# Performance work log

Measured on AMD Instinct MI355X. Metric: run time of the kernel, lower is better.

Reference implementation:

```python
import jax, jax.numpy as jnp
import numpy as np

B, S, D, H, FF = 2, 2048, 1024, 16, 4096
DK = D // H
MAX_SEQ_LEN = 2048
THETA = 10000.0
EPS = 1e-5


def _linear_init(key, out_f, in_f):
    std = (2.0 / (in_f + out_f)) ** 0.5
    return std * jax.random.truncated_normal(key, -3.0, 3.0, (out_f, in_f), dtype=jnp.float32)


def setup_inputs() -> dict:
    key = jax.random.key(0)
    ks = jax.random.split(key, 9)
    x = jax.random.normal(ks[0], (B, S, D), dtype=jnp.float32)
    token_positions = jnp.broadcast_to(jnp.arange(S, dtype=jnp.int32)[None, :], (B, S))
    return {
        "x": x,
        "wq": _linear_init(ks[1], D, D),
        "wk": _linear_init(ks[2], D, D),
        "wv": _linear_init(ks[3], D, D),
        "wo": _linear_init(ks[4], D, D),
        "w1": _linear_init(ks[5], FF, D),
        "w2": _linear_init(ks[6], D, FF),
        "w3": _linear_init(ks[7], FF, D),
        "g1": jnp.ones((D,), dtype=jnp.float32),
        "g2": jnp.ones((D,), dtype=jnp.float32),
        "token_positions": token_positions,
    }


def _rmsnorm(x, g):
    x32 = x.astype(jnp.float32)
    ms = jnp.sqrt(jnp.mean(x32 * x32, axis=-1, keepdims=True) + EPS)
    return ((x32 / ms) * g).astype(x.dtype)


def _rope(x, pos):
    # x: (B, H, S, DK); pos: (B, S)
    inv_freq = 1.0 / THETA ** (jnp.arange(0, DK, 2, dtype=jnp.float32) / DK)  # (DK/2,)
    freqs = pos.astype(jnp.float32)[..., None] * inv_freq  # (B, S, DK/2)
    cos = jnp.cos(freqs)[:, None, :, :]  # (B, 1, S, DK/2) broadcast over heads
    sin = jnp.sin(freqs)[:, None, :, :]
    x_real = x[..., 0::2]
    x_imag = x[..., 1::2]
    rot_real = x_real * cos - x_imag * sin
    rot_imag = x_real * sin + x_imag * cos
    return jnp.stack([rot_real, rot_imag], axis=-1).reshape(x.shape)


def reference(x, wq, wk, wv, wo, w1, w2, w3, g1, g2, token_positions):
    # --- attention sublayer ---
    h = _rmsnorm(x, g1)
    def proj(w):
        y = jnp.einsum('bsd,ed->bse', h, w)
        return y.reshape(B, S, H, DK).transpose(0, 2, 1, 3)  # (B,H,S,DK)
    Q = _rope(proj(wq), token_positions)
    K = _rope(proj(wk), token_positions)
    V = proj(wv)
    scores = jnp.einsum('bhqd,bhkd->bhqk', Q, K)  # (B,H,S,S) full matrix (naive)
    causal = jnp.tril(jnp.ones((S, S), dtype=bool))
    scores = jnp.where(causal, scores, -jnp.inf) / (DK ** 0.5)
    probs = jax.nn.softmax(scores, axis=-1)
    attn = jnp.einsum('bhqk,bhkd->bhqd', probs, V)
    attn = attn.transpose(0, 2, 1, 3).reshape(B, S, D)
    attn = jnp.einsum('bsd,ed->bse', attn, wo)
    y = x + attn
    # --- SwiGLU FFN sublayer ---
    h2 = _rmsnorm(y, g2)
    a = jnp.einsum('bsd,fd->bsf', h2, w1)
    gate = jnp.einsum('bsd,fd->bsf', h2, w3)
    ff = jnp.einsum('bsf,df->bsd', a * jax.nn.sigmoid(a) * gate, w2)
    return y + ff
```

## Files before the change

kernel.cpp:

```cpp
#include <hip/hip_runtime.h>
#include <hip/hip_bf16.h>

#define B_ 2
#define S_ 2048
#define D_ 1024
#define H_ 16
#define DK_ 64
#define FF_ 4096
#define M_ (B_ * S_)

typedef unsigned short u16;
typedef __bf16 bf16x8 __attribute__((ext_vector_type(8)));
typedef float f32x4 __attribute__((ext_vector_type(4)));
typedef u16 u16x4 __attribute__((ext_vector_type(4)));
typedef u16 u16x8 __attribute__((ext_vector_type(8)));

__device__ __forceinline__ u16 f2bf(float f) {
  __bf16 b = (__bf16)f;
  return __builtin_bit_cast(u16, b);
}
__device__ __forceinline__ float bf2f(u16 u) {
  __bf16 b = __builtin_bit_cast(__bf16, u);
  return (float)b;
}

__device__ __forceinline__ void async_lds16(const void* g, void* l) {
  __builtin_amdgcn_global_load_lds(
      (const __attribute__((address_space(1))) unsigned int*)g,
      (__attribute__((address_space(3))) unsigned int*)l, 16, 0, 0);
}

__device__ __forceinline__ void raw_barrier() {
  asm volatile("s_barrier" ::: "memory");
}
#define VMCNT_WAIT(n) asm volatile("s_waitcnt vmcnt(" #n ")" ::: "memory")

__global__ __launch_bounds__(256) void f2b_all(
    const float* __restrict__ wq, const float* __restrict__ wk,
    const float* __restrict__ wv, const float* __restrict__ wo,
    const float* __restrict__ w1, const float* __restrict__ w2,
    const float* __restrict__ w3, u16* __restrict__ wqkvb,
    u16* __restrict__ wob, u16* __restrict__ w1b, u16* __restrict__ w2b,
    u16* __restrict__ w3b) {
  int i4 = blockIdx.x * 256 + threadIdx.x;
  const float* src;
  u16* dst;
  int off;
  if (i4 < 262144) { src = wq; dst = wqkvb; off = i4; }
  else if (i4 < 524288) { src = wk; dst = wqkvb + 1048576; off = i4 - 262144; }
  else if (i4 < 786432) { src = wv; dst = wqkvb + 2097152; off = i4 - 524288; }
  else if (i4 < 1048576) { src = wo; dst = wob; off = i4 - 786432; }
  else if (i4 < 2097152) { src = w1; dst = w1b; off = i4 - 1048576; }
  else if (i4 < 3145728) { src = w2; dst = w2b; off = i4 - 2097152; }
  else { src = w3; dst = w3b; off = i4 - 3145728; }
  float4 v = ((const float4*)src)[off];
  u16x4 o;
  o[0] = f2bf(v.x); o[1] = f2bf(v.y); o[2] = f2bf(v.z); o[3] = f2bf(v.w);
  *(u16x4*)(dst + (size_t)off * 4) = o;
}

__global__ __launch_bounds__(256) void rmsnorm_k(const float* __restrict__ X,
                                                 const float* __restrict__ G,
                                                 u16* __restrict__ Out) {
  const int row = blockIdx.x, tid = threadIdx.x;
  const float4 xv = *(const float4*)(X + (size_t)row * D_ + tid * 4);
  float ss = xv.x * xv.x + xv.y * xv.y + xv.z * xv.z + xv.w * xv.w;
#pragma unroll
  for (int off = 1; off < 64; off <<= 1) ss += __shfl_xor(ss, off);
  __shared__ float red[4];
  if ((tid & 63) == 0) red[tid >> 6] = ss;
  __syncthreads();
  const float tot = red[0] + red[1] + red[2] + red[3];
  const float sc = rsqrtf(tot * (1.0f / D_) + 1e-5f);
  const float4 gv = *(const float4*)(G + tid * 4);
  u16x4 o;
  o[0] = f2bf(xv.x * sc * gv.x);
  o[1] = f2bf(xv.y * sc * gv.y);
  o[2] = f2bf(xv.z * sc * gv.z);
  o[3] = f2bf(xv.w * sc * gv.w);
  *(u16x4*)(Out + (size_t)row * D_ + tid * 4) = o;
}

__global__ __launch_bounds__(256) void rope2_k(unsigned int* __restrict__ Qb,
                                               unsigned int* __restrict__ Kb,
                                               const int* __restrict__ pos) {
  int idx = blockIdx.x * 256 + threadIdx.x;
  unsigned int* buf = Qb;
  float scale = 0.125f;
  if (idx >= 2097152) { buf = Kb; scale = 1.f; idx -= 2097152; }
  const int row = idx >> 9, p = idx & 511;
  const int i = p & 31;
  unsigned int v = buf[(size_t)row * 512 + p];
  const float xr = bf2f((u16)(v & 0xffffu));
  const float xi = bf2f((u16)(v >> 16));
  const float ang =
      (float)pos[row] * __expf(-(float)i * (9.210340371976184f / 32.0f));
  float sn, cs;
  sincosf(ang, &sn, &cs);
  const float orr = (xr * cs - xi * sn) * scale;
  const float oii = (xr * sn + xi * cs) * scale;
  buf[(size_t)row * 512 + p] =
      (unsigned int)f2bf(orr) | ((unsigned int)f2bf(oii) << 16);
}

__global__ __launch_bounds__(256) void transpose_v(const u16* __restrict__ V,
                                                   u16* __restrict__ Vt) {
  __shared__ __align__(16) u16 tile[32][64];
  const int tid = threadIdx.x;
  const int s0 = blockIdx.x * 32, bh = blockIdx.y, b = bh >> 4, h = bh & 15;
  {
    const int sr = tid >> 3, c = tid & 7;
    *(u16x8*)&tile[sr][c * 8] =
        *(const u16x8*)(V + (size_t)(b * S_ + s0 + sr) * D_ + h * DK_ + c * 8);
  }
  __syncthreads();
  {
    const int dk = tid >> 2, cs = tid & 3;
    u16x8 vv;
#pragma unroll
    for (int j = 0; j < 8; ++j) vv[j] = tile[cs * 8 + j][dk];
    *(u16x8*)(Vt + (size_t)(bh * DK_ + dk) * S_ + s0 + cs * 8) = vv;
  }
}

template <int EPI>
__global__ __launch_bounds__(512) void gemm8ph(const u16* __restrict__ A,
                                               const u16* __restrict__ Bw,
                                               void* __restrict__ Cout,
                                               const void* __restrict__ auxp,
                                               int N, int K) {
  constexpr int BM = 256, BN = 256, BK = 64;
  constexpr int CPR = BK / 8;
  constexpr int ACH = BM * CPR;
  __shared__ __align__(16) u16 As[2][BM * BK];
  __shared__ __align__(16) u16 Bs[2][BN * BK];
  const int tid = threadIdx.x, l = tid & 63, w = tid >> 6;
  const int gx = gridDim.x;
  const int nwg = gx * (int)gridDim.y;
  const int id = blockIdx.y * gx + blockIdx.x;
  const int swz = (id & 7) * (nwg >> 3) + (id >> 3);
  const int m0 = (swz / gx) * BM, n0 = (swz % gx) * BN;
  const int wm = (w >> 2) * 128, wn = (w & 3) * 64;
  const int lr = l & 15, lg = l >> 4;

  f32x4 acc[8][4] = {};

  auto STAGE_PART = [&](int bf, int k0, int i0, int i1) {
    for (int i = i0; i < i1; ++i) {
      const int s = i * 512 + tid;
      const int base = i * 512 + w * 64;
      if (base < ACH) {
        const int r = s / CPR, ch = s % CPR;
        async_lds16(A + (size_t)(m0 + r) * K + k0 + ((ch ^ (r & 7)) * 8),
                    (char*)As[bf] + base * 16);
      } else {
        const int s2 = s - ACH;
        const int r = s2 / CPR, ch = s2 % CPR;
        async_lds16(Bw + (size_t)(n0 + r) * K + k0 + ((ch ^ (r & 7)) * 8),
                    (char*)Bs[bf] + (base - ACH) * 16);
      }
    }
  };

  STAGE_PART(0, 0, 0, 8);
  VMCNT_WAIT(0);
  raw_barrier();
  int cur = 0;
  for (int k0 = 0; k0 < K; k0 += BK) {
    const bool more = (k0 + BK) < K;
    bf16x8 bfr[4];
#pragma unroll
    for (int ph = 0; ph < 4; ++ph) {
      const int kk = ph >> 1, iq = ph & 1;
      if (iq == 0) {
#pragma unroll
        for (int j = 0; j < 4; ++j) {
          const int row = wn + j * 16 + lr;
          bfr[j] = *(const bf16x8*)&Bs[cur][row * BK +
                                            (((kk * 4 + lg) ^ (row & 7)) * 8)];
        }
      }
      bf16x8 af[4];
#pragma unroll
      for (int i = 0; i < 4; ++i) {
        const int row = wm + (iq * 4 + i) * 16 + lr;
        af[i] = *(const bf16x8*)&As[cur][row * BK +
                                         (((kk * 4 + lg) ^ (row & 7)) * 8)];
      }
      if (more) {
        if (ph == 0) STAGE_PART(cur ^ 1, k0 + BK, 0, 3);
        else if (ph == 1) STAGE_PART(cur ^ 1, k0 + BK, 3, 6);
        else if (ph == 2) STAGE_PART(cur ^ 1, k0 + BK, 6, 8);
      }
      raw_barrier();
      __builtin_amdgcn_s_setprio(1);
#pragma unroll
      for (int i = 0; i < 4; ++i)
#pragma unroll
        for (int j = 0; j < 4; ++j)
          acc[iq * 4 + i][j] = __builtin_amdgcn_mfma_f32_16x16x32_bf16(
              af[i], bfr[j], acc[iq * 4 + i][j], 0, 0, 0);
      __builtin_amdgcn_s_setprio(0);
      if (ph < 3) raw_barrier();
    }
    if (more) {
      VMCNT_WAIT(0);
      raw_barrier();
    }
    cur ^= 1;
  }

#pragma unroll
  for (int i = 0; i < 8; ++i) {
#pragma unroll
    for (int j = 0; j < 4; ++j) {
#pragma unroll
      for (int t = 0; t < 4; ++t) {
        const int grow = m0 + wm + i * 16 + lg * 4 + t;
        const int gcol = n0 + wn + j * 16 + lr;
        const float v = acc[i][j][t];
        if (EPI == 0) {
          ((u16*)Cout)[(size_t)grow * N + gcol] = f2bf(v);
        } else if (EPI == 2) {
          const size_t idx = (size_t)grow * N + gcol;
          const float av = bf2f(((const u16*)auxp)[idx]);
          const float sw = av / (1.f + __expf(-av));
          ((u16*)Cout)[idx] = f2bf(sw * v);
        } else {
          u16* base = (u16*)Cout + (size_t)(gcol >> 10) * ((size_t)M_ * D_);
          base[(size_t)grow * D_ + (gcol & 1023)] = f2bf(v);
        }
      }
    }
  }
}

template <int BM, int BN, int BK, int EPI>
__global__ __launch_bounds__(512) void gemm2ph(const u16* __restrict__ A,
                                               const u16* __restrict__ Bw,
                                               void* __restrict__ Cout,
                                               const void* __restrict__ auxp,
                                               int N, int K) {
  constexpr int CPR = BK / 8;
  constexpr int ACH = BM * CPR;
  constexpr int TCH = (BM + BN) * CPR;
  constexpr int MR = BM / 32, NR = BN / 64;
  static_assert(TCH / 512 == 8, "vmcnt(8) assumes 8 loads/thread per STAGE");
  __shared__ __align__(16) u16 As[2][BM * BK];
  __shared__ __align__(16) u16 Bs[2][BN * BK];
  const int tid = threadIdx.x, l = tid & 63, w = tid >> 6;
  const int gx = gridDim.x;
  const int nwg = gx * (int)gridDim.y;
  const int id = blockIdx.y * gx + blockIdx.x;
  const int swz = (id & 7) * (nwg >> 3) + (id >> 3);
  const int m0 = (swz / gx) * BM, n0 = (swz % gx) * BN;
  const int wm = (w >> 2) * (BM / 2), wn = (w & 3) * (BN / 4);
  const int lr = l & 15, lg = l >> 4;

  f32x4 acc[MR][NR] = {};

  auto STAGE = [&](int bf, int k0) {
#pragma unroll
    for (int i = 0; i < TCH / 512; ++i) {
      const int s = i * 512 + tid;
      const int base = i * 512 + w * 64;
      if (base < ACH) {
        const int r = s / CPR, ch = s % CPR;
        async_lds16(A + (size_t)(m0 + r) * K + k0 + ((ch ^ (r & 7)) * 8),
                    (char*)As[bf] + base * 16);
      } else {
        const int s2 = s - ACH;
        const int r = s2 / CPR, ch = s2 % CPR;
        async_lds16(Bw + (size_t)(n0 + r) * K + k0 + ((ch ^ (r & 7)) * 8),
                    (char*)Bs[bf] + (base - ACH) * 16);
      }
    }
  };

  STAGE(0, 0);
  int cur = 0;
  for (int k0 = 0; k0 < K; k0 += BK) {
    if (k0 + BK < K) {
      STAGE(cur ^ 1, k0 + BK);
      VMCNT_WAIT(8);
    } else {
      VMCNT_WAIT(0);
    }
    raw_barrier();
#pragma unroll
    for (int kk = 0; kk < BK / 32; ++kk) {
      bf16x8 af[MR], bfr[NR];
#pragma unroll
      for (int i = 0; i < MR; ++i) {
        const int row = wm + i * 16 + lr;
        af[i] = *(const bf16x8*)&As[cur][row * BK +
                                         (((kk * 4 + lg) ^ (row & 7)) * 8)];
      }
#pragma unroll
      for (int j = 0; j < NR; ++j) {
        const int row = wn + j * 16 + lr;
        bfr[j] = *(const bf16x8*)&Bs[cur][row * BK +
                                          (((kk * 4 + lg) ^ (row & 7)) * 8)];
      }
      __builtin_amdgcn_s_setprio(1);
#pragma unroll
      for (int i = 0; i < MR; ++i)
#pragma unroll
        for (int j = 0; j < NR; ++j)
          acc[i][j] = __builtin_amdgcn_mfma_f32_16x16x32_bf16(
              af[i], bfr[j], acc[i][j], 0, 0, 0);
      __builtin_amdgcn_s_setprio(0);
    }
    raw_barrier();
    cur ^= 1;
  }

#pragma unroll
  for (int i = 0; i < MR; ++i) {
#pragma unroll
    for (int j = 0; j < NR; ++j) {
#pragma unroll
      for (int t = 0; t < 4; ++t) {
        const int grow = m0 + wm + i * 16 + lg * 4 + t;
        const int gcol = n0 + wn + j * 16 + lr;
        const float v = acc[i][j][t];
        if (EPI == 0) {
          ((u16*)Cout)[(size_t)grow * N + gcol] = f2bf(v);
        } else if (EPI == 1) {
          const size_t idx = (size_t)grow * N + gcol;
          ((float*)Cout)[idx] = ((const float*)auxp)[idx] + v;
        }
      }
    }
  }
}

__global__ __launch_bounds__(256) void attn_fwd(const u16* __restrict__ Q,
                                                const u16* __restrict__ K,
                                                const u16* __restrict__ Vt,
                                                u16* __restrict__ O) {
  __shared__ __align__(16) u16 Ks[2][64 * 64];
  __shared__ __align__(16) u16 Vs[2][64 * 64];
  __shared__ __align__(16) u16 Ps[4][16 * 72];
  const int tid = threadIdx.x, l = tid & 63, w = tid >> 6;
  const int lr = l & 15, lg = l >> 4;
  const int bid = blockIdx.x;
  const int xcd = bid & 7, i = bid >> 3;
  const int bh = xcd * 4 + (i >> 5);
  const int qx = 31 - (i & 31);
  const int b = bh >> 4, h = bh & 15;
  const int q0w = qx * 64 + w * 16;

  const u16* Kb = K + (size_t)(b * S_) * D_ + h * DK_;
  const u16* Vb = Vt + (size_t)bh * DK_ * S_;

  bf16x8 aq[2];
  {
    const u16* qp = Q + (size_t)(b * S_ + q0w + lr) * D_ + h * DK_ + lg * 8;
    aq[0] = *(const bf16x8*)qp;
    aq[1] = *(const bf16x8*)(qp + 32);
  }
  f32x4 oacc[4] = {};
  float mrow[4], lrow[4];
#pragma unroll
  for (int t = 0; t < 4; ++t) { mrow[t] = -1e30f; lrow[t] = 0.f; }

  u16x8 ones_u;
#pragma unroll
  for (int j = 0; j < 8; ++j) ones_u[j] = 0x3F80;
  const bf16x8 ones = __builtin_bit_cast(bf16x8, ones_u);

  const int ntiles = qx + 1;

  auto STAGE = [&](int bf, int t) {
#pragma unroll
    for (int inst = 0; inst < 2; ++inst) {
      const int s = (w * 2 + inst) * 64 + l;
      const int r = s >> 3, ch = s & 7;
      const int chs = ch ^ (r & 7);
      async_lds16(Kb + (size_t)(t * 64 + r) * D_ + chs * 8,
                  (char*)Ks[bf] + (w * 2 + inst) * 1024);
      async_lds16(Vb + (size_t)r * S_ + t * 64 + chs * 8,
                  (char*)Vs[bf] + (w * 2 + inst) * 1024);
    }
  };

  STAGE(0, 0);
  __syncthreads();
  int cur = 0;
  for (int it = 0; it < ntiles; ++it) {
    if (it + 1 < ntiles) STAGE(cur ^ 1, it + 1);
    f32x4 sf[4];
    __builtin_amdgcn_s_setprio(1);
#pragma unroll
    for (int n = 0; n < 4; ++n) {
      const int kvr = n * 16 + lr;
      f32x4 z = {};
      bf16x8 bk0 = *(const bf16x8*)&Ks[cur][kvr * 64 + ((lg ^ (kvr & 7)) * 8)];
      bf16x8 bk1 =
          *(const bf16x8*)&Ks[cur][kvr * 64 + (((4 + lg) ^ (kvr & 7)) * 8)];
      z = __builtin_amdgcn_mfma_f32_16x16x32_bf16(aq[0], bk0, z, 0, 0, 0);
      z = __builtin_amdgcn_mfma_f32_16x16x32_bf16(aq[1], bk1, z, 0, 0, 0);
      sf[n] = z;
    }
    __builtin_amdgcn_s_setprio(0);
    if (it < qx) {
      float fm[4];
      bool exc = false;
#pragma unroll
      for (int t = 0; t < 4; ++t) {
        fm[t] = fmaxf(fmaxf(sf[0][t], sf[1][t]), fmaxf(sf[2][t], sf[3][t]));
        exc |= fm[t] > mrow[t] + 8.f;
      }
      if (__any(exc)) {
#pragma unroll
        for (int t = 0; t < 4; ++t) {
          float mx = fm[t];
#pragma unroll
          for (int off = 1; off < 16; off <<= 1)
            mx = fmaxf(mx, __shfl_xor(mx, off));
          const float nm = fmaxf(mrow[t], mx);
          const float c = __expf(mrow[t] - nm);
          mrow[t] = nm;
          lrow[t] *= c;
#pragma unroll
          for (int d = 0; d < 4; ++d) oacc[d][t] *= c;
        }
      }
#pragma unroll
      for (int t = 0; t < 4; ++t)
#pragma unroll
        for (int n = 0; n < 4; ++n)
          Ps[w][(lg * 4 + t) * 72 + n * 16 + lr] =
              f2bf(__expf(sf[n][t] - mrow[t]));
    } else {
      const int kv0 = it * 64;
#pragma unroll
      for (int t = 0; t < 4; ++t) {
        const int qrow = q0w + lg * 4 + t;
        float v[4];
#pragma unroll
        for (int n = 0; n < 4; ++n)
          v[n] = (kv0 + n * 16 + lr <= qrow) ? sf[n][t] : -1e30f;
        float mx = fmaxf(fmaxf(v[0], v[1]), fmaxf(v[2], v[3]));
#pragma unroll
        for (int off = 1; off < 16; off <<= 1)
          mx = fmaxf(mx, __shfl_xor(mx, off));
        const float nm = fmaxf(mrow[t], mx);
        const float c = __expf(mrow[t] - nm);
        mrow[t] = nm;
        lrow[t] *= c;
#pragma unroll
        for (int d = 0; d < 4; ++d) oacc[d][t] *= c;
#pragma unroll
        for (int n = 0; n < 4; ++n)
          Ps[w][(lg * 4 + t) * 72 + n * 16 + lr] = f2bf(__expf(v[n] - nm));
      }
    }
    bf16x8 ap0 = *(const bf16x8*)&Ps[w][lr * 72 + lg * 8];
    bf16x8 ap1 = *(const bf16x8*)&Ps[w][lr * 72 + 32 + lg * 8];
    __builtin_amdgcn_s_setprio(1);
    f32x4 zs = {};
    zs = __builtin_amdgcn_mfma_f32_16x16x32_bf16(ap0, ones, zs, 0, 0, 0);
    zs = __builtin_amdgcn_mfma_f32_16x16x32_bf16(ap1, ones, zs, 0, 0, 0);
#pragma unroll
    for (int d = 0; d < 4; ++d) {
      const int row = d * 16 + lr;
      bf16x8 bv0 = *(const bf16x8*)&Vs[cur][row * 64 + ((lg ^ (row & 7)) * 8)];
      bf16x8 bv1 =
          *(const bf16x8*)&Vs[cur][row * 64 + (((4 + lg) ^ (row & 7)) * 8)];
      oacc[d] = __builtin_amdgcn_mfma_f32_16x16x32_bf16(ap0, bv0, oacc[d], 0, 0, 0);
      oacc[d] = __builtin_amdgcn_mfma_f32_16x16x32_bf16(ap1, bv1, oacc[d], 0, 0, 0);
    }
    __builtin_amdgcn_s_setprio(0);
#pragma unroll
    for (int t = 0; t < 4; ++t) lrow[t] += zs[t];
    __syncthreads();
    cur ^= 1;
  }
#pragma unroll
  for (int d = 0; d < 4; ++d) {
#pragma unroll
    for (int t = 0; t < 4; ++t) {
      const size_t idx =
          (size_t)(b * S_ + q0w + lg * 4 + t) * D_ + h * DK_ + d * 16 + lr;
      O[idx] = f2bf(oacc[d][t] / lrow[t]);
    }
  }
}

extern "C" void kernel_launch(void* const* d_in, const int* in_sizes, int n_in,
                              void* d_out, int out_size, void* d_ws,
                              size_t ws_size, hipStream_t stream) {
  (void)in_sizes; (void)n_in; (void)out_size; (void)ws_size;
  const float* x = (const float*)d_in[0];
  const float* wq = (const float*)d_in[1];
  const float* wk = (const float*)d_in[2];
  const float* wv = (const float*)d_in[3];
  const float* wo = (const float*)d_in[4];
  const float* w1 = (const float*)d_in[5];
  const float* w2 = (const float*)d_in[6];
  const float* w3 = (const float*)d_in[7];
  const float* g1 = (const float*)d_in[8];
  const float* g2 = (const float*)d_in[9];
  const int* tp = (const int*)d_in[10];
  float* out = (float*)d_out;

  char* ws = (char*)d_ws;
  const size_t MB = 1024u * 1024u;
  u16* wqkvb = (u16*)(ws + 0 * MB);
  u16* wob = (u16*)(ws + 6 * MB);
  u16* w1b = (u16*)(ws + 8 * MB);
  u16* w2b = (u16*)(ws + 16 * MB);
  u16* w3b = (u16*)(ws + 24 * MB);
  u16* hb  = (u16*)(ws + 32 * MB);
  float* yb = (float*)(ws + 40 * MB);
  u16* h2b = (u16*)(ws + 56 * MB);
  u16* Qb  = (u16*)(ws + 64 * MB);
  u16* Kb  = (u16*)(ws + 72 * MB);
  u16* Vb  = (u16*)(ws + 80 * MB);
  u16* Vtb = (u16*)(ws + 88 * MB);
  u16* ab  = (u16*)(ws + 64 * MB);
  u16* ffb = (u16*)(ws + 96 * MB);
  u16* aob = hb;

  f2b_all<<<16384, 256, 0, stream>>>(wq, wk, wv, wo, w1, w2, w3, wqkvb, wob,
                                     w1b, w2b, w3b);

  rmsnorm_k<<<4096, 256, 0, stream>>>(x, g1, hb);

  gemm8ph<3><<<dim3(12, 16), 512, 0, stream>>>(hb, wqkvb, Qb, nullptr, 3072,
                                               1024);

  rope2_k<<<16384, 256, 0, stream>>>((unsigned int*)Qb, (unsigned int*)Kb, tp);
  transpose_v<<<dim3(64, 32), 256, 0, stream>>>(Vb, Vtb);

  attn_fwd<<<1024, 256, 0, stream>>>(Qb, Kb, Vtb, aob);

  gemm2ph<128, 128, 128, 1><<<dim3(8, 32), 512, 0, stream>>>(aob, wob, yb, x,
                                                             1024, 1024);
  rmsnorm_k<<<4096, 256, 0, stream>>>(yb, g2, h2b);

  gemm8ph<0><<<dim3(16, 16), 512, 0, stream>>>(h2b, w1b, ab, nullptr, 4096,
                                               1024);
  gemm8ph<2><<<dim3(16, 16), 512, 0, stream>>>(h2b, w3b, ffb, ab, 4096, 1024);
  gemm2ph<128, 128, 128, 1><<<dim3(8, 32), 512, 0, stream>>>(ffb, w2b, out, yb,
                                                             1024, 4096);
}
```

Before: 284.9 us.

## Fuse W1/W3 FFN GEMMs via row-interleaved weights and relax attention sync

Interleaves the bf16 rows of w1 and w3 into one weight matrix so that a single GEMM of width 8192 computes both projections. Its epilogue pairs adjacent columns with a lane shuffle and writes silu(a)*gate directly. This removes the separate w1 GEMM launch and the write and re-read of the intermediate activation buffer. The attention kernel also replaces its full __syncthreads with a vmcnt wait plus raw barrier placed after issuing the next tile's async loads, so the prefetch can overlap. Half the lanes are idle during the fused epilogue stores, and the stores become strided.

```diff
diff --git a/kernel.cpp b/kernel.cpp
--- a/kernel.cpp
+++ b/kernel.cpp
@@ -40,23 +40,27 @@
     const float* __restrict__ wv, const float* __restrict__ wo,
     const float* __restrict__ w1, const float* __restrict__ w2,
     const float* __restrict__ w3, u16* __restrict__ wqkvb,
-    u16* __restrict__ wob, u16* __restrict__ w1b, u16* __restrict__ w2b,
-    u16* __restrict__ w3b) {
+    u16* __restrict__ wob, u16* __restrict__ wb13, u16* __restrict__ w2b) {
   int i4 = blockIdx.x * 256 + threadIdx.x;
   const float* src;
   u16* dst;
-  int off;
-  if (i4 < 262144) { src = wq; dst = wqkvb; off = i4; }
-  else if (i4 < 524288) { src = wk; dst = wqkvb + 1048576; off = i4 - 262144; }
-  else if (i4 < 786432) { src = wv; dst = wqkvb + 2097152; off = i4 - 524288; }
-  else if (i4 < 1048576) { src = wo; dst = wob; off = i4 - 786432; }
-  else if (i4 < 2097152) { src = w1; dst = w1b; off = i4 - 1048576; }
-  else if (i4 < 3145728) { src = w2; dst = w2b; off = i4 - 2097152; }
-  else { src = w3; dst = w3b; off = i4 - 3145728; }
+  int off, oo;
+  if (i4 < 262144) { src = wq; dst = wqkvb; off = i4; oo = off; }
+  else if (i4 < 524288) { src = wk; dst = wqkvb + 1048576; off = i4 - 262144; oo = off; }
+  else if (i4 < 786432) { src = wv; dst = wqkvb + 2097152; off = i4 - 524288; oo = off; }
+  else if (i4 < 1048576) { src = wo; dst = wob; off = i4 - 786432; oo = off; }
+  else if (i4 < 2097152) {
+    src = w1; dst = wb13; off = i4 - 1048576;
+    oo = ((off >> 8) * 2) * 256 + (off & 255);
+  } else if (i4 < 3145728) { src = w2; dst = w2b; off = i4 - 2097152; oo = off; }
+  else {
+    src = w3; dst = wb13; off = i4 - 3145728;
+    oo = ((off >> 8) * 2 + 1) * 256 + (off & 255);
+  }
   float4 v = ((const float4*)src)[off];
   u16x4 o;
   o[0] = f2bf(v.x); o[1] = f2bf(v.y); o[2] = f2bf(v.z); o[3] = f2bf(v.w);
-  *(u16x4*)(dst + (size_t)off * 4) = o;
+  *(u16x4*)(dst + (size_t)oo * 4) = o;
 }
 
 __global__ __launch_bounds__(256) void rmsnorm_k(const float* __restrict__ X,
@@ -221,14 +225,15 @@
         const float v = acc[i][j][t];
         if (EPI == 0) {
           ((u16*)Cout)[(size_t)grow * N + gcol] = f2bf(v);
-        } else if (EPI == 2) {
-          const size_t idx = (size_t)grow * N + gcol;
-          const float av = bf2f(((const u16*)auxp)[idx]);
-          const float sw = av / (1.f + __expf(-av));
-          ((u16*)Cout)[idx] = f2bf(sw * v);
-        } else {
+        } else if (EPI == 3) {
           u16* base = (u16*)Cout + (size_t)(gcol >> 10) * ((size_t)M_ * D_);
           base[(size_t)grow * D_ + (gcol & 1023)] = f2bf(v);
+        } else {
+          const float pv = __shfl_xor(v, 1);
+          if (!(lr & 1)) {
+            const float sw = v / (1.f + __expf(-v)) * pv;
+            ((u16*)Cout)[(size_t)grow * FF_ + (gcol >> 1)] = f2bf(sw);
+          }
         }
       }
     }
@@ -386,10 +391,15 @@
   };
 
   STAGE(0, 0);
-  __syncthreads();
   int cur = 0;
   for (int it = 0; it < ntiles; ++it) {
-    if (it + 1 < ntiles) STAGE(cur ^ 1, it + 1);
+    if (it + 1 < ntiles) {
+      STAGE(cur ^ 1, it + 1);
+      VMCNT_WAIT(4);
+    } else {
+      VMCNT_WAIT(0);
+    }
+    raw_barrier();
     f32x4 sf[4];
     __builtin_amdgcn_s_setprio(1);
 #pragma unroll
@@ -475,7 +485,7 @@
     __builtin_amdgcn_s_setprio(0);
 #pragma unroll
     for (int t = 0; t < 4; ++t) lrow[t] += zs[t];
-    __syncthreads();
+    raw_barrier();
     cur ^= 1;
   }
 #pragma unroll
@@ -509,23 +519,21 @@
   char* ws = (char*)d_ws;
   const size_t MB = 1024u * 1024u;
   u16* wqkvb = (u16*)(ws + 0 * MB);
-  u16* wob = (u16*)(ws + 6 * MB);
-  u16* w1b = (u16*)(ws + 8 * MB);
-  u16* w2b = (u16*)(ws + 16 * MB);
-  u16* w3b = (u16*)(ws + 24 * MB);
-  u16* hb  = (u16*)(ws + 32 * MB);
+  u16* wob  = (u16*)(ws + 6 * MB);
+  u16* wb13 = (u16*)(ws + 8 * MB);
+  u16* w2b  = (u16*)(ws + 24 * MB);
+  u16* hb   = (u16*)(ws + 32 * MB);
   float* yb = (float*)(ws + 40 * MB);
-  u16* h2b = (u16*)(ws + 56 * MB);
-  u16* Qb  = (u16*)(ws + 64 * MB);
-  u16* Kb  = (u16*)(ws + 72 * MB);
-  u16* Vb  = (u16*)(ws + 80 * MB);
-  u16* Vtb = (u16*)(ws + 88 * MB);
-  u16* ab  = (u16*)(ws + 64 * MB);
-  u16* ffb = (u16*)(ws + 96 * MB);
-  u16* aob = hb;
+  u16* h2b  = (u16*)(ws + 56 * MB);
+  u16* Qb   = (u16*)(ws + 64 * MB);
+  u16* Kb   = (u16*)(ws + 72 * MB);
+  u16* Vb   = (u16*)(ws + 80 * MB);
+  u16* Vtb  = (u16*)(ws + 88 * MB);
+  u16* ffb  = (u16*)(ws + 96 * MB);
+  u16* aob  = hb;
 
   f2b_all<<<16384, 256, 0, stream>>>(wq, wk, wv, wo, w1, w2, w3, wqkvb, wob,
-                                     w1b, w2b, w3b);
+                                     wb13, w2b);
 
   rmsnorm_k<<<4096, 256, 0, stream>>>(x, g1, hb);
 
@@ -541,9 +549,8 @@
                                                              1024, 1024);
   rmsnorm_k<<<4096, 256, 0, stream>>>(yb, g2, h2b);
 
-  gemm8ph<0><<<dim3(16, 16), 512, 0, stream>>>(h2b, w1b, ab, nullptr, 4096,
+  gemm8ph<4><<<dim3(32, 16), 512, 0, stream>>>(h2b, wb13, ffb, nullptr, 8192,
                                                1024);
-  gemm8ph<2><<<dim3(16, 16), 512, 0, stream>>>(h2b, w3b, ffb, ab, 4096, 1024);
   gemm2ph<128, 128, 128, 1><<<dim3(8, 32), 512, 0, stream>>>(ffb, w2b, out, yb,
                                                              1024, 4096);
 }
```

Measured after the change: 293.1 us. 2.9% more time.
